# Optimization experiments

Measured on AMD Instinct MI355X. Metric: run time of the kernel, lower is better.

The kernel has to match this reference:

```python
import jax, jax.numpy as jnp
import numpy as np

BST_DEPTH = 6
NB_SPLIT = 2**BST_DEPTH - 1          # 63 internal (split) nodes
NB_NODES = 2**(BST_DEPTH + 1) - 1    # 127 total nodes (heap layout)
SPLIT = np.arange(NB_SPLIT)
DESC_L = 2 * SPLIT + 1               # left children of split nodes
DESC_R = 2 * SPLIT + 2               # right children of split nodes


def setup_inputs() -> dict:
    key = jax.random.key(0)
    kx, ka = jax.random.split(key)
    x = jax.random.normal(kx, (131072, 512), dtype=jnp.float32)
    A = jax.random.uniform(ka, (NB_SPLIT, 512), dtype=jnp.float32)  # torch.rand init
    return {"x": x, "A": A}


def _compute_q(x, A):
    # XA[:, t] is the split score of internal node t; XA == XA[:, split_nodes]
    XA = x @ A.T                                         # [N, nb_split]
    q = jnp.ones((x.shape[0], NB_NODES), dtype=XA.dtype)  # [N, nb_nodes]
    # Seed children of each split node. NOTE: sequential semantics matter —
    # the right-child write reads q[:, SPLIT] AFTER the left-child write
    # (odd-indexed split nodes were just updated), matching torch in-place ops.
    q = q.at[:, DESC_L].set(jnp.minimum(q[:, SPLIT], XA))
    q = q.at[:, DESC_R].set(jnp.minimum(q[:, SPLIT], -XA))
    # Propagate the running min from parents down the tree, one sweep per level.
    for _ in range(BST_DEPTH):
        q = q.at[:, DESC_L].set(jnp.minimum(q[:, DESC_L], q[:, SPLIT]))
        q = q.at[:, DESC_R].set(jnp.minimum(q[:, DESC_R], q[:, SPLIT]))
    return q


def reference(x, A):
    q = _compute_q(x, A)
    z = jnp.clip(q, 0.0, 1.0)  # pruned=False: no QP pruning branch
    return z
```

## Files before the change

### kernel.cpp

```cpp
#include <hip/hip_runtime.h>
#include <hip/hip_bf16.h>
#include <cstdint>

#define KD 512
#define BM 128
#define NT 512
#define NSPLIT 63
#define NNODES 127
#define B_OFF 32768

typedef __attribute__((ext_vector_type(8))) short bf16x8;
typedef __attribute__((ext_vector_type(4))) float f32x4;

#define MFMA_B16(a, b, c) __builtin_amdgcn_mfma_f32_16x16x32_bf16(a, b, c, 0, 0, 0)
#define SCHED_FENCE() __builtin_amdgcn_sched_barrier(0)

static __device__ __forceinline__ unsigned short f2bf(float f) {
    return __builtin_bit_cast(unsigned short, __float2bfloat16(f));
}
static __device__ __forceinline__ float bf2f(unsigned short h) {
    return __builtin_bit_cast(float, (unsigned)h << 16);
}
static __device__ __forceinline__ unsigned pack2(float f0, float f1) {
    return (unsigned)f2bf(f0) | ((unsigned)f2bf(f1) << 16);
}

static __device__ __forceinline__ void cvt8(f32x4 a, f32x4 b, bf16x8& hi, bf16x8& lo) {
    const unsigned short h0 = f2bf(a[0]), h1 = f2bf(a[1]), h2 = f2bf(a[2]), h3 = f2bf(a[3]);
    const unsigned short h4 = f2bf(b[0]), h5 = f2bf(b[1]), h6 = f2bf(b[2]), h7 = f2bf(b[3]);
    uint4 H = make_uint4((unsigned)h0 | ((unsigned)h1 << 16), (unsigned)h2 | ((unsigned)h3 << 16),
                         (unsigned)h4 | ((unsigned)h5 << 16), (unsigned)h6 | ((unsigned)h7 << 16));
    uint4 L = make_uint4(pack2(a[0] - bf2f(h0), a[1] - bf2f(h1)),
                         pack2(a[2] - bf2f(h2), a[3] - bf2f(h3)),
                         pack2(b[0] - bf2f(h4), b[1] - bf2f(h5)),
                         pack2(b[2] - bf2f(h6), b[3] - bf2f(h7)));
    hi = __builtin_bit_cast(bf16x8, H);
    lo = __builtin_bit_cast(bf16x8, L);
}

static __device__ __forceinline__ void gload_lds16(const void* g, void* l) {
    __builtin_amdgcn_global_load_lds(
        (const __attribute__((address_space(1))) unsigned int*)g,
        (__attribute__((address_space(3))) unsigned int*)l, 16, 0, 0);
}

template<int N> static __device__ __forceinline__ void vmwait() {
    if constexpr (N == 2) asm volatile("s_waitcnt vmcnt(2)" ::: "memory");
    else                  asm volatile("s_waitcnt vmcnt(0)" ::: "memory");
}

template<int T>
static __device__ __forceinline__ void tree_walk16(float qt, const float* __restrict__ srow,
                                                   float* __restrict__ zrow, int part16) {
    const float s  = srow[T];
    const float ql = fminf(qt, s);
    const float qr = fminf(qt, -s);
    if (((2 * T + 1) >> 3) == part16) zrow[2 * T + 1] = fminf(fmaxf(ql, 0.f), 1.f);
    if (((2 * T + 2) >> 3) == part16) zrow[2 * T + 2] = fminf(fmaxf(qr, 0.f), 1.f);
    if constexpr (2 * T + 1 < NSPLIT) tree_walk16<2 * T + 1>(ql, srow, zrow, part16);
    if constexpr (2 * T + 2 < NSPLIT) tree_walk16<2 * T + 2>(qr, srow, zrow, part16);
}

__global__ __launch_bounds__(256)
void lt_prep(const float* __restrict__ A, unsigned short* __restrict__ ws) {
    const int gid = blockIdx.x * 256 + threadIdx.x;
    const int row = gid >> 7;
    const int c4  = (gid & 127) << 2;
    f32x4 v = (f32x4)(0.f);
    if (row < NSPLIT)
        v = *reinterpret_cast<const f32x4*>(A + (size_t)row * KD + c4);
    const unsigned short h0 = f2bf(v[0]), h1 = f2bf(v[1]), h2 = f2bf(v[2]), h3 = f2bf(v[3]);
    uint2 hv = make_uint2((unsigned)h0 | ((unsigned)h1 << 16),
                          (unsigned)h2 | ((unsigned)h3 << 16));
    uint2 lv = make_uint2(pack2(v[0] - bf2f(h0), v[1] - bf2f(h1)),
                          pack2(v[2] - bf2f(h2), v[3] - bf2f(h3)));
    *reinterpret_cast<uint2*>(ws + row * KD + c4)         = hv;
    *reinterpret_cast<uint2*>(ws + 32768 + row * KD + c4) = lv;
}

template<int T>
static __device__ __forceinline__ void tiles(
        const float* xsrc, const unsigned short* bsrc,
        unsigned char* xw, unsigned char* bB, int bdoff,
        int va_off, int bo, f32x4 (&acc)[4]) {
    if constexpr (T + 1 < 16)
        gload_lds16(bsrc + (T + 1) * 32, bB + ((T + 1) & 1) * 8192 + bdoff);
    SCHED_FENCE();
    const unsigned char* xbf = xw + (T & 1) * 2048;
    f32x4 va = *reinterpret_cast<const f32x4*>(xbf + va_off);
    f32x4 vb = *reinterpret_cast<const f32x4*>(xbf + (va_off ^ 16));
    const unsigned char* bb = bB + (T & 1) * 8192;
    bf16x8 bh0 = *reinterpret_cast<const bf16x8*>(bb + bo);
    bf16x8 bh1 = *reinterpret_cast<const bf16x8*>(bb + bo + 1024);
    bf16x8 bh2 = *reinterpret_cast<const bf16x8*>(bb + bo + 2048);
    bf16x8 bh3 = *reinterpret_cast<const bf16x8*>(bb + bo + 3072);
    asm volatile("s_waitcnt lgkmcnt(0)" ::: "memory");
    SCHED_FENCE();
    if constexpr (T + 2 < 16) {
        gload_lds16(xsrc + (T + 2) * 32, xw + (T & 1) * 2048);
        gload_lds16(xsrc + (T + 2) * 32 + 8 * KD, xw + (T & 1) * 2048 + 1024);
    }
    SCHED_FENCE();
    bf16x8 ah, al;
    cvt8(va, vb, ah, al);
    acc[0] = MFMA_B16(ah, bh0, acc[0]);
    acc[1] = MFMA_B16(ah, bh1, acc[1]);
    acc[2] = MFMA_B16(ah, bh2, acc[2]);
    acc[3] = MFMA_B16(ah, bh3, acc[3]);
    acc[0] = MFMA_B16(al, bh0, acc[0]);
    acc[1] = MFMA_B16(al, bh1, acc[1]);
    acc[2] = MFMA_B16(al, bh2, acc[2]);
    acc[3] = MFMA_B16(al, bh3, acc[3]);
    bf16x8 bl0 = *reinterpret_cast<const bf16x8*>(bb + 4096 + bo);
    bf16x8 bl1 = *reinterpret_cast<const bf16x8*>(bb + 4096 + bo + 1024);
    bf16x8 bl2 = *reinterpret_cast<const bf16x8*>(bb + 4096 + bo + 2048);
    bf16x8 bl3 = *reinterpret_cast<const bf16x8*>(bb + 4096 + bo + 3072);
    acc[0] = MFMA_B16(ah, bl0, acc[0]);
    acc[1] = MFMA_B16(ah, bl1, acc[1]);
    acc[2] = MFMA_B16(ah, bl2, acc[2]);
    acc[3] = MFMA_B16(ah, bl3, acc[3]);
    if constexpr (T + 1 < 16) {
        SCHED_FENCE();
        vmwait<(T + 2 < 16) ? 2 : 0>();
        SCHED_FENCE();
        __builtin_amdgcn_s_barrier();
        tiles<T + 1>(xsrc, bsrc, xw, bB, bdoff, va_off, bo, acc);
    }
}

__global__ __launch_bounds__(NT, 6)
void lt_mfma9(const float* __restrict__ x, const unsigned short* __restrict__ ws,
              float* __restrict__ out) {
    __shared__ __align__(16) unsigned char lds[49152];
    unsigned char* bB = lds + B_OFF;

    const int tid  = threadIdx.x;
    const int wave = tid >> 6;
    const int lane = tid & 63;
    const int fr   = lane & 15;
    const int g    = lane >> 4;
    const int r0   = blockIdx.x * BM;

    unsigned char* xw = lds + wave * 4096;
    const float* xsrc = x + (size_t)(r0 + wave * 16 + (lane >> 3)) * KD
                          + (((lane & 7) ^ ((lane >> 3) & 7)) << 2);
    const int p  = wave >> 2;
    const int qq = wave & 3;
    {
    }
    const int brow = qq * 16 + (lane >> 2);
    const unsigned short* bsrc = ws + p * 32768 + brow * KD
                                    + (((lane & 3) ^ (brow & 3)) << 3);
    const int bdoff = p * 4096 + qq * 1024;
    const int va_off = (fr << 7) + (((g << 1) ^ (fr & 7)) << 4);
    const int bo     = (fr << 6) + ((g ^ (fr & 3)) << 4);

    f32x4 acc[4];
#pragma unroll
    for (int j = 0; j < 4; ++j) acc[j] = (f32x4)(0.f);

    gload_lds16(bsrc, bB + bdoff);
    gload_lds16(xsrc, xw);
    gload_lds16(xsrc + 8 * KD, xw + 1024);
    gload_lds16(xsrc + 32, xw + 2048);
    gload_lds16(xsrc + 32 + 8 * KD, xw + 3072);
    SCHED_FENCE();
    vmwait<2>();
    SCHED_FENCE();
    __builtin_amdgcn_s_barrier();

    tiles<0>(xsrc, bsrc, xw, bB, bdoff, va_off, bo, acc);

    float* warea = reinterpret_cast<float*>(xw);
    float* zw    = warea + 260;
    const int o      = lane >> 4;
    const int part16 = lane & 15;

#pragma unroll
    for (int s = 0; s < 4; ++s) {
        if (g == s) {
#pragma unroll
            for (int nf = 0; nf < 4; ++nf)
#pragma unroll
                for (int rg = 0; rg < 4; ++rg)
                    warea[rg * 65 + nf * 16 + fr] = acc[nf][rg];
        }
        const float* srow = warea + o * 65;
        float* zrow = zw + o * NNODES;
        if (part16 == 0) zrow[0] = 1.f;
        tree_walk16<0>(1.f, srow, zrow, part16);

        float* og = out + (size_t)(r0 + wave * 16 + s * 4) * NNODES;
#pragma unroll
        for (int j = 0; j < 2; ++j) {
            const int idx = j * 64 + lane;
            if (idx < 127)
                *reinterpret_cast<f32x4*>(og + idx * 4) =
                    *reinterpret_cast<const f32x4*>(zw + idx * 4);
        }
    }
}

extern "C" void kernel_launch(void* const* d_in, const int* in_sizes, int n_in,
                              void* d_out, int out_size, void* d_ws, size_t ws_size,
                              hipStream_t stream) {
    const float* x = (const float*)d_in[0];
    const float* A = (const float*)d_in[1];
    float* out = (float*)d_out;
    unsigned short* ws = (unsigned short*)d_ws;
    const int nrows = in_sizes[0] / KD;
    lt_prep<<<dim3(32), dim3(256), 0, stream>>>(A, ws);
    lt_mfma9<<<dim3(nrows / BM), dim3(NT), 0, stream>>>(x, ws, out);
}
```

Measured before the change: 96.85 us.

## Fuse A bf16 split-conversion into main kernel and drop prep launch

```diff
diff --git a/kernel.cpp b/kernel.cpp
--- a/kernel.cpp
+++ b/kernel.cpp
@@ -7,7 +7,8 @@
 #define NT 512
 #define NSPLIT 63
 #define NNODES 127
-#define B_OFF 32768
+#define BH_OFF 32768
+#define BL_OFF 40960
 
 typedef __attribute__((ext_vector_type(8))) short bf16x8;
 typedef __attribute__((ext_vector_type(4))) float f32x4;
@@ -45,8 +46,9 @@
 }
 
 template<int N> static __device__ __forceinline__ void vmwait() {
-    if constexpr (N == 2) asm volatile("s_waitcnt vmcnt(2)" ::: "memory");
-    else                  asm volatile("s_waitcnt vmcnt(0)" ::: "memory");
+    if constexpr (N == 4)      asm volatile("s_waitcnt vmcnt(4)" ::: "memory");
+    else if constexpr (N == 2) asm volatile("s_waitcnt vmcnt(2)" ::: "memory");
+    else                       asm volatile("s_waitcnt vmcnt(0)" ::: "memory");
 }
 
 template<int T>
@@ -61,78 +63,83 @@
     if constexpr (2 * T + 2 < NSPLIT) tree_walk16<2 * T + 2>(qr, srow, zrow, part16);
 }
 
-__global__ __launch_bounds__(256)
-void lt_prep(const float* __restrict__ A, unsigned short* __restrict__ ws) {
-    const int gid = blockIdx.x * 256 + threadIdx.x;
-    const int row = gid >> 7;
-    const int c4  = (gid & 127) << 2;
-    f32x4 v = (f32x4)(0.f);
-    if (row < NSPLIT)
-        v = *reinterpret_cast<const f32x4*>(A + (size_t)row * KD + c4);
-    const unsigned short h0 = f2bf(v[0]), h1 = f2bf(v[1]), h2 = f2bf(v[2]), h3 = f2bf(v[3]);
-    uint2 hv = make_uint2((unsigned)h0 | ((unsigned)h1 << 16),
-                          (unsigned)h2 | ((unsigned)h3 << 16));
-    uint2 lv = make_uint2(pack2(v[0] - bf2f(h0), v[1] - bf2f(h1)),
-                          pack2(v[2] - bf2f(h2), v[3] - bf2f(h3)));
-    *reinterpret_cast<uint2*>(ws + row * KD + c4)         = hv;
-    *reinterpret_cast<uint2*>(ws + 32768 + row * KD + c4) = lv;
+static __device__ __forceinline__ void write_B(unsigned char* lds, int brow, int sl,
+                                               bool bvalid, f32x4 b0, f32x4 b1) {
+    if (!bvalid) { b0 = (f32x4)(0.f); b1 = (f32x4)(0.f); }
+    bf16x8 hi, lo;
+    cvt8(b0, b1, hi, lo);
+    *reinterpret_cast<bf16x8*>(lds + BH_OFF + brow * 128 + sl * 16) = hi;
+    *reinterpret_cast<bf16x8*>(lds + BL_OFF + brow * 128 + sl * 16) = lo;
 }
 
 template<int T>
 static __device__ __forceinline__ void tiles(
-        const float* xsrc, const unsigned short* bsrc,
-        unsigned char* xw, unsigned char* bB, int bdoff,
-        int va_off, int bo, f32x4 (&acc)[4]) {
-    if constexpr (T + 1 < 16)
-        gload_lds16(bsrc + (T + 1) * 32, bB + ((T + 1) & 1) * 8192 + bdoff);
-    SCHED_FENCE();
+        const float* xsrc, unsigned char* xw, unsigned char* lds,
+        const float* ag, bool bvalid, int brow, int sl,
+        int va_off, int fr, int g, f32x4 (&acc)[4], f32x4& bn0, f32x4& bn1) {
+    if constexpr ((T & 1) == 0 && T > 0) {
+        SCHED_FENCE();
+        __builtin_amdgcn_s_barrier();
+        write_B(lds, brow, sl, bvalid, bn0, bn1);
+        asm volatile("s_waitcnt lgkmcnt(0)" ::: "memory");
+        __builtin_amdgcn_s_barrier();
+        SCHED_FENCE();
+        if constexpr (T / 2 + 1 < 8) {
+            if (bvalid) {
+                bn0 = *reinterpret_cast<const f32x4*>(ag + (T / 2 + 1) * 64);
+                bn1 = *reinterpret_cast<const f32x4*>(ag + (T / 2 + 1) * 64 + 4);
+            }
+        }
+        SCHED_FENCE();
+    }
+    if constexpr (T + 1 < 16) {
+        unsigned char* nb = xw + ((T + 1) & 1) * 2048;
+        gload_lds16(xsrc + (T + 1) * 32, nb);
+        gload_lds16(xsrc + (T + 1) * 32 + 8 * KD, nb + 1024);
+    }
+    SCHED_FENCE();
+    vmwait<((T & 1) == 0 && T <= 12) ? 4 : ((T == 15) ? 0 : 2)>();
+    SCHED_FENCE();
+
     const unsigned char* xbf = xw + (T & 1) * 2048;
     f32x4 va = *reinterpret_cast<const f32x4*>(xbf + va_off);
     f32x4 vb = *reinterpret_cast<const f32x4*>(xbf + (va_off ^ 16));
-    const unsigned char* bb = bB + (T & 1) * 8192;
-    bf16x8 bh0 = *reinterpret_cast<const bf16x8*>(bb + bo);
-    bf16x8 bh1 = *reinterpret_cast<const bf16x8*>(bb + bo + 1024);
-    bf16x8 bh2 = *reinterpret_cast<const bf16x8*>(bb + bo + 2048);
-    bf16x8 bh3 = *reinterpret_cast<const bf16x8*>(bb + bo + 3072);
-    asm volatile("s_waitcnt lgkmcnt(0)" ::: "memory");
-    SCHED_FENCE();
-    if constexpr (T + 2 < 16) {
-        gload_lds16(xsrc + (T + 2) * 32, xw + (T & 1) * 2048);
-        gload_lds16(xsrc + (T + 2) * 32 + 8 * KD, xw + (T & 1) * 2048 + 1024);
-    }
-    SCHED_FENCE();
     bf16x8 ah, al;
     cvt8(va, vb, ah, al);
-    acc[0] = MFMA_B16(ah, bh0, acc[0]);
-    acc[1] = MFMA_B16(ah, bh1, acc[1]);
-    acc[2] = MFMA_B16(ah, bh2, acc[2]);
-    acc[3] = MFMA_B16(ah, bh3, acc[3]);
-    acc[0] = MFMA_B16(al, bh0, acc[0]);
-    acc[1] = MFMA_B16(al, bh1, acc[1]);
-    acc[2] = MFMA_B16(al, bh2, acc[2]);
-    acc[3] = MFMA_B16(al, bh3, acc[3]);
-    bf16x8 bl0 = *reinterpret_cast<const bf16x8*>(bb + 4096 + bo);
-    bf16x8 bl1 = *reinterpret_cast<const bf16x8*>(bb + 4096 + bo + 1024);
-    bf16x8 bl2 = *reinterpret_cast<const bf16x8*>(bb + 4096 + bo + 2048);
-    bf16x8 bl3 = *reinterpret_cast<const bf16x8*>(bb + 4096 + bo + 3072);
-    acc[0] = MFMA_B16(ah, bl0, acc[0]);
-    acc[1] = MFMA_B16(ah, bl1, acc[1]);
-    acc[2] = MFMA_B16(ah, bl2, acc[2]);
-    acc[3] = MFMA_B16(ah, bl3, acc[3]);
-    if constexpr (T + 1 < 16) {
-        SCHED_FENCE();
-        vmwait<(T + 2 < 16) ? 2 : 0>();
-        SCHED_FENCE();
-        __builtin_amdgcn_s_barrier();
-        tiles<T + 1>(xsrc, bsrc, xw, bB, bdoff, va_off, bo, acc);
-    }
+
+    const int m   = fr & 7;
+    const int bof = fr * 128 + ((((T & 1) * 4) + g) ^ m) * 16;
+    const unsigned char* bh = lds + BH_OFF + bof;
+    bf16x8 b0 = *reinterpret_cast<const bf16x8*>(bh);
+    bf16x8 b1 = *reinterpret_cast<const bf16x8*>(bh + 2048);
+    bf16x8 b2 = *reinterpret_cast<const bf16x8*>(bh + 4096);
+    bf16x8 b3 = *reinterpret_cast<const bf16x8*>(bh + 6144);
+    acc[0] = MFMA_B16(ah, b0, acc[0]);
+    acc[1] = MFMA_B16(ah, b1, acc[1]);
+    acc[2] = MFMA_B16(ah, b2, acc[2]);
+    acc[3] = MFMA_B16(ah, b3, acc[3]);
+    acc[0] = MFMA_B16(al, b0, acc[0]);
+    acc[1] = MFMA_B16(al, b1, acc[1]);
+    acc[2] = MFMA_B16(al, b2, acc[2]);
+    acc[3] = MFMA_B16(al, b3, acc[3]);
+    const unsigned char* blp = lds + BL_OFF + bof;
+    b0 = *reinterpret_cast<const bf16x8*>(blp);
+    b1 = *reinterpret_cast<const bf16x8*>(blp + 2048);
+    b2 = *reinterpret_cast<const bf16x8*>(blp + 4096);
+    b3 = *reinterpret_cast<const bf16x8*>(blp + 6144);
+    acc[0] = MFMA_B16(ah, b0, acc[0]);
+    acc[1] = MFMA_B16(ah, b1, acc[1]);
+    acc[2] = MFMA_B16(ah, b2, acc[2]);
+    acc[3] = MFMA_B16(ah, b3, acc[3]);
+
+    if constexpr (T + 1 < 16)
+        tiles<T + 1>(xsrc, xw, lds, ag, bvalid, brow, sl, va_off, fr, g, acc, bn0, bn1);
 }
 
 __global__ __launch_bounds__(NT, 6)
-void lt_mfma9(const float* __restrict__ x, const unsigned short* __restrict__ ws,
-              float* __restrict__ out) {
+void lt_mfma11(const float* __restrict__ x, const float* __restrict__ A,
+               float* __restrict__ out) {
     __shared__ __align__(16) unsigned char lds[49152];
-    unsigned char* bB = lds + B_OFF;
 
     const int tid  = threadIdx.x;
     const int wave = tid >> 6;
@@ -144,32 +151,35 @@
     unsigned char* xw = lds + wave * 4096;
     const float* xsrc = x + (size_t)(r0 + wave * 16 + (lane >> 3)) * KD
                           + (((lane & 7) ^ ((lane >> 3) & 7)) << 2);
-    const int p  = wave >> 2;
-    const int qq = wave & 3;
-    {
-    }
-    const int brow = qq * 16 + (lane >> 2);
-    const unsigned short* bsrc = ws + p * 32768 + brow * KD
-                                    + (((lane & 3) ^ (brow & 3)) << 3);
-    const int bdoff = p * 4096 + qq * 1024;
-    const int va_off = (fr << 7) + (((g << 1) ^ (fr & 7)) << 4);
-    const int bo     = (fr << 6) + ((g ^ (fr & 3)) << 4);
+    const int brow = tid >> 3;
+    const int bq   = tid & 7;
+    const int sl   = bq ^ (brow & 7);
+    const bool bvalid = brow < NSPLIT;
+    const float* ag = A + (size_t)brow * KD + bq * 8;
+    const int va_off = (fr << 7) + (((2 * g) ^ (fr & 7)) << 4);
 
     f32x4 acc[4];
 #pragma unroll
     for (int j = 0; j < 4; ++j) acc[j] = (f32x4)(0.f);
 
-    gload_lds16(bsrc, bB + bdoff);
+    f32x4 bn0 = (f32x4)(0.f), bn1 = (f32x4)(0.f);
+    if (bvalid) {
+        bn0 = *reinterpret_cast<const f32x4*>(ag);
+        bn1 = *reinterpret_cast<const f32x4*>(ag + 4);
+    }
     gload_lds16(xsrc, xw);
     gload_lds16(xsrc + 8 * KD, xw + 1024);
-    gload_lds16(xsrc + 32, xw + 2048);
-    gload_lds16(xsrc + 32 + 8 * KD, xw + 3072);
-    SCHED_FENCE();
-    vmwait<2>();
-    SCHED_FENCE();
+    SCHED_FENCE();
+    write_B(lds, brow, sl, bvalid, bn0, bn1);
+    asm volatile("s_waitcnt lgkmcnt(0)" ::: "memory");
     __builtin_amdgcn_s_barrier();
-
-    tiles<0>(xsrc, bsrc, xw, bB, bdoff, va_off, bo, acc);
+    if (bvalid) {
+        bn0 = *reinterpret_cast<const f32x4*>(ag + 64);
+        bn1 = *reinterpret_cast<const f32x4*>(ag + 68);
+    }
+    SCHED_FENCE();
+
+    tiles<0>(xsrc, xw, lds, ag, bvalid, brow, sl, va_off, fr, g, acc, bn0, bn1);
 
     float* warea = reinterpret_cast<float*>(xw);
     float* zw    = warea + 260;
@@ -207,8 +217,7 @@
     const float* x = (const float*)d_in[0];
     const float* A = (const float*)d_in[1];
     float* out = (float*)d_out;
-    unsigned short* ws = (unsigned short*)d_ws;
     const int nrows = in_sizes[0] / KD;
-    lt_prep<<<dim3(32), dim3(256), 0, stream>>>(A, ws);
-    lt_mfma9<<<dim3(nrows / BM), dim3(NT), 0, stream>>>(x, ws, out);
-}
+    const int grid = nrows / BM;
+    lt_mfma11<<<dim3(grid), dim3(NT), 0, stream>>>(x, A, out);
+}
```

Result: faster. 94.81 us (-2.1%).
